# Performance work log

Measured on AMD Instinct MI355X. Metric: run time of the kernel, lower is better.

Reference implementation:

```python
import jax, jax.numpy as jnp
import numpy as np

DIM = 2048
NUM_EXPERTS = 8
EXPERT_DIM = 1024
B, S = 4, 2048


def setup_inputs() -> dict:
    key = jax.random.key(0)
    ks = jax.random.split(key, 8)
    sd = lambda fan_in: 1.0 / np.sqrt(fan_in)  # lecun-normal-ish init scale
    x = jax.random.normal(ks[0], (B, S, DIM), dtype=jnp.float32)
    Wr = jax.random.normal(ks[1], (DIM, NUM_EXPERTS), dtype=jnp.float32) * sd(DIM)
    br = jnp.zeros((NUM_EXPERTS,), dtype=jnp.float32)
    Wu = jax.random.normal(ks[2], (NUM_EXPERTS, DIM, EXPERT_DIM), dtype=jnp.float32) * sd(DIM)
    bu = jnp.zeros((NUM_EXPERTS, EXPERT_DIM), dtype=jnp.float32)
    Wd = jax.random.normal(ks[3], (NUM_EXPERTS, EXPERT_DIM, DIM), dtype=jnp.float32) * sd(EXPERT_DIM)
    bd = jnp.zeros((NUM_EXPERTS, DIM), dtype=jnp.float32)
    return {"x": x, "Wr": Wr, "br": br, "Wu": Wu, "bu": bu, "Wd": Wd, "bd": bd}


def reference(x, Wr, br, Wu, bu, Wd, bd):
    # Router: softmax over experts. x: [b,s,d]
    router_probs = jax.nn.softmax(jnp.einsum('bsd,de->bse', x, Wr) + br, axis=-1)
    # All experts as grouped GEMMs (e = expert axis).
    h = jnp.einsum('bsd,edf->bsef', x, Wu) + bu          # [b,s,e,expert_dim]
    h = jax.nn.gelu(h)                                    # tanh-approx gelu (flax default)
    y = jnp.einsum('bsef,efd->bsed', h, Wd) + bd          # [b,s,e,dim]
    out = jnp.einsum('bsed,bse->bsd', y, router_probs)    # router-weighted sum
    return out + x
```

## Files before the change

kernel.cpp:

```cpp
#include <hip/hip_runtime.h>
#include <stdint.h>

#define DIM   2048
#define NEXP  8
#define EDIM  1024
#define NTOK  8192

using bf16x8 = __attribute__((ext_vector_type(8))) short;
using f32x4  = __attribute__((ext_vector_type(4))) float;
using u16x2  = __attribute__((ext_vector_type(2))) unsigned short;

typedef __attribute__((address_space(3))) void lds_void_t;
typedef const __attribute__((address_space(1))) void gbl_void_t;

__device__ static inline void load_lds16(const void* g, void* l) {
    __builtin_amdgcn_global_load_lds((gbl_void_t*)g, (lds_void_t*)l, 16, 0, 0);
}

__device__ static inline unsigned short f2b(float x) {
    union { float f; unsigned u; } v; v.f = x;
    unsigned r = v.u + 0x7fffu + ((v.u >> 16) & 1u);
    return (unsigned short)(r >> 16);
}

__device__ static inline float gelu_f(float x) {
    float u = 0.7978845608028654f * x * (1.0f + 0.044715f * x * x);
    u = fminf(fmaxf(u, -15.0f), 15.0f);
    float e = __expf(2.0f * u);
    float th = (e - 1.0f) / (e + 1.0f);
    return 0.5f * x * (1.0f + th);
}

__global__ __launch_bounds__(256)
void transpose_cast(const float* __restrict__ in, unsigned short* __restrict__ out,
                    int R, int C) {
    __shared__ float tile[64][65];
    const size_t slab = (size_t)blockIdx.z * R * C;
    in  += slab;
    out += slab;
    const int r0 = blockIdx.y * 64;
    const int c0 = blockIdx.x * 64;
    const int tx = threadIdx.x & 63;
    const int tw = threadIdx.x >> 6;
    #pragma unroll
    for (int i = 0; i < 16; ++i)
        tile[tw * 16 + i][tx] = in[(size_t)(r0 + tw * 16 + i) * C + c0 + tx];
    __syncthreads();
    const int rp = (threadIdx.x & 31) * 2;
    const int cy = threadIdx.x >> 5;
    #pragma unroll
    for (int j = 0; j < 8; ++j) {
        const int c = cy + j * 8;
        u16x2 v;
        v.x = f2b(tile[rp][c]);
        v.y = f2b(tile[rp + 1][c]);
        *(u16x2*)&out[(size_t)(c0 + c) * R + r0 + rp] = v;
    }
}

__global__ __launch_bounds__(256)
void router_convert(const float* __restrict__ x, const float* __restrict__ Wr,
                    const float* __restrict__ br, unsigned short* __restrict__ xb,
                    float* __restrict__ probs) {
    const int t   = blockIdx.x;
    const int tid = threadIdx.x;
    const float* xr = x + (size_t)t * DIM;
    const float4* Wr4 = (const float4*)Wr;
    float s[NEXP];
    #pragma unroll
    for (int e = 0; e < NEXP; ++e) s[e] = 0.f;
    for (int j = tid; j < DIM; j += 256) {
        float v = xr[j];
        xb[(size_t)t * DIM + j] = f2b(v);
        const float4 w0 = Wr4[j * 2];
        const float4 w1 = Wr4[j * 2 + 1];
        s[0] += v * w0.x; s[1] += v * w0.y; s[2] += v * w0.z; s[3] += v * w0.w;
        s[4] += v * w1.x; s[5] += v * w1.y; s[6] += v * w1.z; s[7] += v * w1.w;
    }
    #pragma unroll
    for (int e = 0; e < NEXP; ++e)
        #pragma unroll
        for (int off = 32; off > 0; off >>= 1) s[e] += __shfl_down(s[e], off);
    __shared__ float part[4][NEXP];
    const int wave = tid >> 6, lane = tid & 63;
    if (lane == 0) {
        #pragma unroll
        for (int e = 0; e < NEXP; ++e) part[wave][e] = s[e];
    }
    __syncthreads();
    if (tid == 0) {
        float l[NEXP], mx = -1e30f;
        #pragma unroll
        for (int e = 0; e < NEXP; ++e) {
            l[e] = part[0][e] + part[1][e] + part[2][e] + part[3][e] + br[e];
            mx = fmaxf(mx, l[e]);
        }
        float sum = 0.f;
        #pragma unroll
        for (int e = 0; e < NEXP; ++e) { l[e] = __expf(l[e] - mx); sum += l[e]; }
        const float inv = 1.f / sum;
        #pragma unroll
        for (int e = 0; e < NEXP; ++e) probs[t * NEXP + e] = l[e] * inv;
    }
}

#define VMWAIT(n) asm volatile("s_waitcnt vmcnt(" #n ")" ::: "memory")
#define SCHEDB()  __builtin_amdgcn_sched_barrier(0)
#define PHASE_SYNC1() do { SCHEDB(); asm volatile("" ::: "memory"); \
    __builtin_amdgcn_s_barrier(); \
    asm volatile("s_waitcnt lgkmcnt(0)" ::: "memory"); SCHEDB(); } while (0)
#define PHASE_SYNC2() do { SCHEDB(); asm volatile("" ::: "memory"); \
    __builtin_amdgcn_s_barrier(); \
    asm volatile("" ::: "memory"); SCHEDB(); } while (0)

#define STAGE_A(bufc, rho, koff) do { \
    load_lds16(srcA + (size_t)((rho) * 128) * K + (koff),      dstA + (bufc) * 16384 + (rho) * 8192); \
    load_lds16(srcA + (size_t)((rho) * 128 + 64) * K + (koff), dstA + (bufc) * 16384 + (rho) * 8192 + 4096); \
} while (0)

#define STAGE_B(bufc, rho, koff) do { \
    load_lds16(srcB + (size_t)((rho) * 128) * K + (koff),      dstB + (bufc) * 16384 + (rho) * 8192); \
    load_lds16(srcB + (size_t)((rho) * 128 + 64) * K + (koff), dstB + (bufc) * 16384 + (rho) * 8192 + 4096); \
} while (0)

#define DSR128(dst, addr, IMM) \
    asm volatile("ds_read_b128 %0, %1 offset:%2" : "=v"(dst) : "v"(addr), "n"(IMM))

#define RD_B(bb) do { \
    DSR128(bfr[0][0], bAddr0, (bb)*32768 + 0);    DSR128(bfr[0][1], bAddr1, (bb)*32768 + 0); \
    DSR128(bfr[1][0], bAddr0, (bb)*32768 + 2048); DSR128(bfr[1][1], bAddr1, (bb)*32768 + 2048); \
    DSR128(bfr[2][0], bAddr0, (bb)*32768 + 4096); DSR128(bfr[2][1], bAddr1, (bb)*32768 + 4096); \
    DSR128(bfr[3][0], bAddr0, (bb)*32768 + 6144); DSR128(bfr[3][1], bAddr1, (bb)*32768 + 6144); \
} while (0)

#define RD_A2(dst, I0, bb) do { \
    DSR128(dst[0][0], aAddr0, (bb)*32768 + (I0)*2048);       DSR128(dst[0][1], aAddr1, (bb)*32768 + (I0)*2048); \
    DSR128(dst[1][0], aAddr0, (bb)*32768 + ((I0)+1)*2048);   DSR128(dst[1][1], aAddr1, (bb)*32768 + ((I0)+1)*2048); \
} while (0)

#define MFMA_Q(i0, AF) do { \
    __builtin_amdgcn_s_setprio(1); \
    _Pragma("unroll") for (int ii = 0; ii < 2; ++ii) \
    _Pragma("unroll") for (int u = 0; u < 2; ++u) \
    _Pragma("unroll") for (int j = 0; j < 4; ++j) \
        acc[(i0) + ii][j] = __builtin_amdgcn_mfma_f32_16x16x32_bf16(AF[ii][u], bfr[j][u], acc[(i0) + ii][j], 0, 0, 0); \
    __builtin_amdgcn_s_setprio(0); \
} while (0)

#define KTILE(bb, ISS1, ISS2, ISS3, ISS4, VMW) do { \
    bf16x8 bfr[4][2], aA[2][2], aB[2][2]; \
     \
    RD_B(bb); RD_A2(aA, 0, bb); \
    ISS1; \
    PHASE_SYNC1(); \
    MFMA_Q(0, aA); \
    PHASE_SYNC2(); \
     \
    RD_A2(aB, 2, bb); RD_A2(aA, 4, bb); \
    ISS2; \
    PHASE_SYNC1(); \
    MFMA_Q(2, aB); \
    PHASE_SYNC2(); \
     \
    RD_A2(aB, 6, bb); \
    ISS3; \
    PHASE_SYNC1(); \
    MFMA_Q(4, aA); \
    PHASE_SYNC2(); \
     \
    ISS4; \
    VMW; \
    PHASE_SYNC1(); \
    MFMA_Q(6, aB); \
    PHASE_SYNC2(); \
} while (0)

template <int MODE>
__global__ __launch_bounds__(512, 2)
void gemm_bt(const unsigned short* __restrict__ A,
             const unsigned short* __restrict__ Bt,
             int M, int N, int K,
             const float* __restrict__ probs,
             const float* __restrict__ bias,
             const float* __restrict__ xres,
             void* __restrict__ Cout)
{
    __shared__ unsigned short As[2][16384];
    __shared__ unsigned short Bs[2][16384];

    const int tid  = threadIdx.x;
    const int wave = tid >> 6;
    const int lane = tid & 63;
    const int wm   = wave >> 2;
    const int wn   = wave & 3;
    const int m    = lane & 15;
    const int q    = lane >> 4;
    const int xsw  = m & 7;

    const int nwg = gridDim.x * gridDim.y;
    int bid = blockIdx.y * gridDim.x + blockIdx.x;
    if (!(nwg & 7)) bid = (bid & 7) * (nwg >> 3) + (bid >> 3);
    const int row0 = (bid / gridDim.x) * 256;
    const int col0 = (bid % gridDim.x) * 256;

    const int rloc = tid >> 3;
    const int kc   = (tid & 7) ^ (rloc & 7);
    const unsigned short* srcA = A  + (size_t)(row0 + rloc) * K + kc * 8;
    const unsigned short* srcB = Bt + (size_t)(col0 + rloc) * K + kc * 8;
    unsigned short* dstA = &As[0][0] + tid * 8;
    unsigned short* dstB = &Bs[0][0] + tid * 8;

    const int arow = (wm * 128 + m) * 64;
    const int brow = (wn * 64  + m) * 64;
    int ko[2];
    #pragma unroll
    for (int u = 0; u < 2; ++u) ko[u] = ((u * 4 + q) ^ xsw) * 8;
    const unsigned ldsAbase = (unsigned)(uintptr_t)&As[0][0];
    const unsigned ldsBbase = (unsigned)(uintptr_t)&Bs[0][0];
    const unsigned aAddr0 = ldsAbase + (unsigned)((arow + ko[0]) * 2);
    const unsigned aAddr1 = ldsAbase + (unsigned)((arow + ko[1]) * 2);
    const unsigned bAddr0 = ldsBbase + (unsigned)((brow + ko[0]) * 2);
    const unsigned bAddr1 = ldsBbase + (unsigned)((brow + ko[1]) * 2);

    f32x4 acc[8][4];
    #pragma unroll
    for (int i = 0; i < 8; ++i)
        #pragma unroll
        for (int j = 0; j < 4; ++j)
            acc[i][j] = (f32x4){0.f, 0.f, 0.f, 0.f};

    const int NT = K >> 6;

    STAGE_B(0, 0, 0);  STAGE_B(0, 1, 0);  STAGE_A(0, 0, 0);  STAGE_A(0, 1, 0);
    STAGE_B(1, 0, 64); STAGE_B(1, 1, 64); STAGE_A(1, 0, 64);
    VMWAIT(6);
    SCHEDB();
    asm volatile("" ::: "memory");
    __builtin_amdgcn_s_barrier();
    asm volatile("" ::: "memory");
    SCHEDB();

    for (int t = 0; t + 3 < NT; t += 2) {
        const size_t k1 = (size_t)(t + 1) * 64;
        const size_t k2 = (size_t)(t + 2) * 64;
        const size_t k3 = (size_t)(t + 3) * 64;
        KTILE(0, STAGE_A(1, 1, k1), STAGE_B(0, 0, k2), STAGE_B(0, 1, k2), STAGE_A(0, 0, k2), VMWAIT(6));
        KTILE(1, STAGE_A(0, 1, k2), STAGE_B(1, 0, k3), STAGE_B(1, 1, k3), STAGE_A(1, 0, k3), VMWAIT(6));
    }
    {
        const size_t kl = (size_t)(NT - 1) * 64;
        KTILE(0, STAGE_A(1, 1, kl), (void)0, (void)0, (void)0, VMWAIT(0));
        KTILE(1, (void)0, (void)0, (void)0, (void)0, (void)0);
    }

    if (MODE == 1) {
        unsigned short* H = (unsigned short*)Cout;
        const int e = col0 >> 10;
        float bv[4];
        #pragma unroll
        for (int j = 0; j < 4; ++j) bv[j] = bias[col0 + wn * 64 + j * 16 + m];
        #pragma unroll
        for (int i = 0; i < 8; ++i) {
            #pragma unroll
            for (int r = 0; r < 4; ++r) {
                const int rowg = row0 + wm * 128 + i * 16 + q * 4 + r;
                const float p = probs[rowg * NEXP + e];
                #pragma unroll
                for (int j = 0; j < 4; ++j) {
                    const int colg = col0 + wn * 64 + j * 16 + m;
                    float v = acc[i][j][r] + bv[j];
                    H[(size_t)rowg * N + colg] = f2b(gelu_f(v) * p);
                }
            }
        }
    } else {
        float* O = (float*)Cout;
        float bdv[4][NEXP];
        #pragma unroll
        for (int j = 0; j < 4; ++j) {
            const int colg = col0 + wn * 64 + j * 16 + m;
            #pragma unroll
            for (int e = 0; e < NEXP; ++e) bdv[j][e] = bias[e * DIM + colg];
        }
        #pragma unroll
        for (int i = 0; i < 8; ++i) {
            #pragma unroll
            for (int r = 0; r < 4; ++r) {
                const int rowg = row0 + wm * 128 + i * 16 + q * 4 + r;
                float p[NEXP];
                *(float4*)&p[0] = *(const float4*)&probs[rowg * NEXP];
                *(float4*)&p[4] = *(const float4*)&probs[rowg * NEXP + 4];
                #pragma unroll
                for (int j = 0; j < 4; ++j) {
                    const int colg = col0 + wn * 64 + j * 16 + m;
                    float v = acc[i][j][r];
                    #pragma unroll
                    for (int e = 0; e < NEXP; ++e) v += p[e] * bdv[j][e];
                    v += xres[(size_t)rowg * DIM + colg];
                    O[(size_t)rowg * N + colg] = v;
                }
            }
        }
    }
}

extern "C" void kernel_launch(void* const* d_in, const int* in_sizes, int n_in,
                              void* d_out, int out_size, void* d_ws, size_t ws_size,
                              hipStream_t stream) {
    const float* x  = (const float*)d_in[0];
    const float* Wr = (const float*)d_in[1];
    const float* br = (const float*)d_in[2];
    const float* Wu = (const float*)d_in[3];
    const float* bu = (const float*)d_in[4];
    const float* Wd = (const float*)d_in[5];
    const float* bd = (const float*)d_in[6];
    float* out = (float*)d_out;

    char* ws = (char*)d_ws;
    unsigned short* xb    = (unsigned short*)(ws);
    unsigned short* WuT   = (unsigned short*)(ws + 33554432);
    unsigned short* WdT   = (unsigned short*)(ws + 67108864);
    float*          probs = (float*)(ws + 100663296);
    unsigned short* h     = (unsigned short*)(ws + 100925440);

    transpose_cast<<<dim3(EDIM / 64, DIM / 64, NEXP), 256, 0, stream>>>(Wu, WuT, DIM, EDIM);
    transpose_cast<<<dim3(DIM / 64, (NEXP * EDIM) / 64, 1), 256, 0, stream>>>(Wd, WdT, NEXP * EDIM, DIM);
    router_convert<<<NTOK, 256, 0, stream>>>(x, Wr, br, xb, probs);
    gemm_bt<1><<<dim3((NEXP * EDIM) / 256, NTOK / 256), 512, 0, stream>>>(
        xb, WuT, NTOK, NEXP * EDIM, DIM, probs, bu, nullptr, h);
    gemm_bt<2><<<dim3(DIM / 256, NTOK / 256), 512, 0, stream>>>(
        h, WdT, NTOK, DIM, NEXP * EDIM, probs, bd, x, out);
}
```

Before: 755.1 us.

## Software-pipeline LDS fragment reads across k-tiles with double-buffered B registers

Restructures the GEMM k-tile loop so the B fragments and first A fragments for the next k-tile are read from LDS during the last MFMA phase of the current tile, using two register sets for B. Full lgkmcnt(0) waits are replaced by partial lgkmcnt waits so LDS reads overlap MFMA work. This is meant to hide LDS read latency at phase boundaries. The cost is higher VGPR pressure at 512 threads with 2 blocks per CU, plus more fragile wait-count bookkeeping.

```diff
diff --git a/kernel.cpp b/kernel.cpp
--- a/kernel.cpp
+++ b/kernel.cpp
@@ -104,14 +104,13 @@
     }
 }
 
-#define VMWAIT(n) asm volatile("s_waitcnt vmcnt(" #n ")" ::: "memory")
-#define SCHEDB()  __builtin_amdgcn_sched_barrier(0)
-#define PHASE_SYNC1() do { SCHEDB(); asm volatile("" ::: "memory"); \
-    __builtin_amdgcn_s_barrier(); \
-    asm volatile("s_waitcnt lgkmcnt(0)" ::: "memory"); SCHEDB(); } while (0)
-#define PHASE_SYNC2() do { SCHEDB(); asm volatile("" ::: "memory"); \
-    __builtin_amdgcn_s_barrier(); \
-    asm volatile("" ::: "memory"); SCHEDB(); } while (0)
+#define VMWAIT(n)   asm volatile("s_waitcnt vmcnt(" #n ")" ::: "memory")
+#define LGKMWAIT(n) asm volatile("s_waitcnt lgkmcnt(" #n ")" ::: "memory")
+#define SCHEDB()    __builtin_amdgcn_sched_barrier(0)
+#define BARRIER()   do { asm volatile("" ::: "memory"); \
+    __builtin_amdgcn_s_barrier(); asm volatile("" ::: "memory"); } while (0)
+#define PS1(W) do { SCHEDB(); BARRIER(); W; SCHEDB(); } while (0)
+#define PS2()  do { SCHEDB(); BARRIER(); SCHEDB(); } while (0)
 
 #define STAGE_A(bufc, rho, koff) do { \
     load_lds16(srcA + (size_t)((rho) * 128) * K + (koff),      dstA + (bufc) * 16384 + (rho) * 8192); \
@@ -126,11 +125,11 @@
 #define DSR128(dst, addr, IMM) \
     asm volatile("ds_read_b128 %0, %1 offset:%2" : "=v"(dst) : "v"(addr), "n"(IMM))
 
-#define RD_B(bb) do { \
-    DSR128(bfr[0][0], bAddr0, (bb)*32768 + 0);    DSR128(bfr[0][1], bAddr1, (bb)*32768 + 0); \
-    DSR128(bfr[1][0], bAddr0, (bb)*32768 + 2048); DSR128(bfr[1][1], bAddr1, (bb)*32768 + 2048); \
-    DSR128(bfr[2][0], bAddr0, (bb)*32768 + 4096); DSR128(bfr[2][1], bAddr1, (bb)*32768 + 4096); \
-    DSR128(bfr[3][0], bAddr0, (bb)*32768 + 6144); DSR128(bfr[3][1], bAddr1, (bb)*32768 + 6144); \
+#define RD_B(BF, bb) do { \
+    DSR128(BF[0][0], bAddr0, (bb)*32768 + 0);    DSR128(BF[0][1], bAddr1, (bb)*32768 + 0); \
+    DSR128(BF[1][0], bAddr0, (bb)*32768 + 2048); DSR128(BF[1][1], bAddr1, (bb)*32768 + 2048); \
+    DSR128(BF[2][0], bAddr0, (bb)*32768 + 4096); DSR128(BF[2][1], bAddr1, (bb)*32768 + 4096); \
+    DSR128(BF[3][0], bAddr0, (bb)*32768 + 6144); DSR128(BF[3][1], bAddr1, (bb)*32768 + 6144); \
 } while (0)
 
 #define RD_A2(dst, I0, bb) do { \
@@ -138,41 +137,45 @@
     DSR128(dst[1][0], aAddr0, (bb)*32768 + ((I0)+1)*2048);   DSR128(dst[1][1], aAddr1, (bb)*32768 + ((I0)+1)*2048); \
 } while (0)
 
-#define MFMA_Q(i0, AF) do { \
+#define RDN(BF, nb) do { RD_B(BF, nb); RD_A2(aA, 0, nb); } while (0)
+
+#define MFMA_Q(i0, AF, BF) do { \
     __builtin_amdgcn_s_setprio(1); \
     _Pragma("unroll") for (int ii = 0; ii < 2; ++ii) \
     _Pragma("unroll") for (int u = 0; u < 2; ++u) \
     _Pragma("unroll") for (int j = 0; j < 4; ++j) \
-        acc[(i0) + ii][j] = __builtin_amdgcn_mfma_f32_16x16x32_bf16(AF[ii][u], bfr[j][u], acc[(i0) + ii][j], 0, 0, 0); \
+        acc[(i0) + ii][j] = __builtin_amdgcn_mfma_f32_16x16x32_bf16(AF[ii][u], BF[j][u], acc[(i0) + ii][j], 0, 0, 0); \
     __builtin_amdgcn_s_setprio(0); \
 } while (0)
 
-#define KTILE(bb, ISS1, ISS2, ISS3, ISS4, VMW) do { \
-    bf16x8 bfr[4][2], aA[2][2], aB[2][2]; \
+#define KTILE(bb, BC, ISS1, ISS2, ISS3, ISS4, VMW, RDNEXT, W4) do { \
      \
-    RD_B(bb); RD_A2(aA, 0, bb); \
+    RD_A2(aB, 2, bb); \
     ISS1; \
-    PHASE_SYNC1(); \
-    MFMA_Q(0, aA); \
-    PHASE_SYNC2(); \
+    PS1(LGKMWAIT(4)); \
+    MFMA_Q(0, aA, BC); \
+    PS2(); \
      \
-    RD_A2(aB, 2, bb); RD_A2(aA, 4, bb); \
+    RD_A2(aA, 4, bb); \
     ISS2; \
-    PHASE_SYNC1(); \
-    MFMA_Q(2, aB); \
-    PHASE_SYNC2(); \
+    PS1(LGKMWAIT(4)); \
+    MFMA_Q(2, aB, BC); \
+    PS2(); \
      \
     RD_A2(aB, 6, bb); \
     ISS3; \
-    PHASE_SYNC1(); \
-    MFMA_Q(4, aA); \
-    PHASE_SYNC2(); \
+    PS1(LGKMWAIT(4)); \
+    MFMA_Q(4, aA, BC); \
+    PS2(); \
      \
     ISS4; \
     VMW; \
-    PHASE_SYNC1(); \
-    MFMA_Q(6, aB); \
-    PHASE_SYNC2(); \
+    SCHEDB(); BARRIER(); \
+    RDNEXT; \
+    W4; \
+    SCHEDB(); \
+    MFMA_Q(6, aB, BC); \
+    PS2(); \
 } while (0)
 
 template <int MODE>
@@ -229,28 +232,32 @@
         for (int j = 0; j < 4; ++j)
             acc[i][j] = (f32x4){0.f, 0.f, 0.f, 0.f};
 
+    bf16x8 bfr0[4][2], bfr1[4][2], aA[2][2], aB[2][2];
+
     const int NT = K >> 6;
 
     STAGE_B(0, 0, 0);  STAGE_B(0, 1, 0);  STAGE_A(0, 0, 0);  STAGE_A(0, 1, 0);
     STAGE_B(1, 0, 64); STAGE_B(1, 1, 64); STAGE_A(1, 0, 64);
     VMWAIT(6);
-    SCHEDB();
-    asm volatile("" ::: "memory");
-    __builtin_amdgcn_s_barrier();
-    asm volatile("" ::: "memory");
+    SCHEDB(); BARRIER();
+    RDN(bfr0, 0);
     SCHEDB();
 
     for (int t = 0; t + 3 < NT; t += 2) {
         const size_t k1 = (size_t)(t + 1) * 64;
         const size_t k2 = (size_t)(t + 2) * 64;
         const size_t k3 = (size_t)(t + 3) * 64;
-        KTILE(0, STAGE_A(1, 1, k1), STAGE_B(0, 0, k2), STAGE_B(0, 1, k2), STAGE_A(0, 0, k2), VMWAIT(6));
-        KTILE(1, STAGE_A(0, 1, k2), STAGE_B(1, 0, k3), STAGE_B(1, 1, k3), STAGE_A(1, 0, k3), VMWAIT(6));
+        KTILE(0, bfr0, STAGE_A(1, 1, k1), STAGE_B(0, 0, k2), STAGE_B(0, 1, k2),
+              STAGE_A(0, 0, k2), VMWAIT(6), RDN(bfr1, 1), LGKMWAIT(12));
+        KTILE(1, bfr1, STAGE_A(0, 1, k2), STAGE_B(1, 0, k3), STAGE_B(1, 1, k3),
+              STAGE_A(1, 0, k3), VMWAIT(6), RDN(bfr0, 0), LGKMWAIT(12));
     }
     {
         const size_t kl = (size_t)(NT - 1) * 64;
-        KTILE(0, STAGE_A(1, 1, kl), (void)0, (void)0, (void)0, VMWAIT(0));
-        KTILE(1, (void)0, (void)0, (void)0, (void)0, (void)0);
+        KTILE(0, bfr0, STAGE_A(1, 1, kl), (void)0, (void)0, (void)0,
+              VMWAIT(0), RDN(bfr1, 1), LGKMWAIT(12));
+        KTILE(1, bfr1, (void)0, (void)0, (void)0, (void)0,
+              (void)0, (void)0, LGKMWAIT(0));
     }
 
     if (MODE == 1) {
```

Result: slower. 1.021 ms (+35.2%).
